# Optimization experiments

Measured on AMD Instinct MI355X. Metric: run time of the kernel, lower is better.

The kernel has to match this reference:

```python
import jax, jax.numpy as jnp
import numpy as np

H = 128
T = 120
F_IN = 180
BN_EPS = 1e-5
LEAKY_SLOPE = 0.01


def _lstm_layer(x, wih, whh, bih, bhh):
    """Single LSTM layer. x: (B,T,D); wih:(4H,D), whh:(4H,H). PyTorch gate order i,f,g,o."""
    B = x.shape[0]
    # Precompute input projections for all timesteps: (B,T,4H)
    x_proj = jnp.einsum('btd,gd->btg', x, wih) + bih + bhh
    x_proj = jnp.transpose(x_proj, (1, 0, 2))  # (T,B,4H) for scan over time
    h0 = jnp.zeros((B, H), dtype=x.dtype)
    c0 = jnp.zeros((B, H), dtype=x.dtype)

    def step(carry, xt):
        h, c = carry
        gates = xt + h @ whh.T  # (B,4H)
        i, f, g, o = jnp.split(gates, 4, axis=-1)
        i = jax.nn.sigmoid(i)
        f = jax.nn.sigmoid(f)
        g = jnp.tanh(g)
        o = jax.nn.sigmoid(o)
        c = f * c + i * g
        h = o * jnp.tanh(c)
        return (h, c), h

    (_, _), hs = jax.lax.scan(step, (h0, c0), x_proj)  # hs: (T,B,H)
    return jnp.transpose(hs, (1, 0, 2))  # (B,T,H)


def setup_inputs() -> dict:
    key = jax.random.key(0)
    ks = jax.random.split(key, 16)
    B = 2048
    s = 0.1  # keep activations in a stable range
    inp = {
        'x': jax.random.normal(ks[0], (B, F_IN, T), jnp.float32),
        'fc_w': jax.random.normal(ks[1], (H, F_IN), jnp.float32) * s,
        'fc_b': jax.random.normal(ks[2], (H,), jnp.float32) * s,
        'bn_g': jax.random.uniform(ks[3], (H,), jnp.float32, 0.5, 1.5),
        'bn_b': jax.random.normal(ks[4], (H,), jnp.float32) * s,
        'bn_mean': jax.random.normal(ks[5], (H,), jnp.float32) * s,
        'bn_var': jax.random.uniform(ks[6], (H,), jnp.float32, 0.5, 1.5),
        'wih0': jax.random.normal(ks[7], (4 * H, H), jnp.float32) * s,
        'whh0': jax.random.normal(ks[8], (4 * H, H), jnp.float32) * s,
        'bih0': jax.random.normal(ks[9], (4 * H,), jnp.float32) * s,
        'bhh0': jax.random.normal(ks[10], (4 * H,), jnp.float32) * s,
        'wih1': jax.random.normal(ks[11], (4 * H, H), jnp.float32) * s,
        'whh1': jax.random.normal(ks[12], (4 * H, H), jnp.float32) * s,
        'bih1': jax.random.normal(ks[13], (4 * H,), jnp.float32) * s,
        'bhh1': jax.random.normal(ks[14], (4 * H,), jnp.float32) * s,
    }
    return inp


def reference(x, fc_w, fc_b, bn_g, bn_b, bn_mean, bn_var,
              wih0, whh0, bih0, bhh0, wih1, whh1, bih1, bhh1):
    # x.reshape(-1,180,120).permute(0,2,1) -> (B,120,180)
    h = jnp.transpose(x.reshape(-1, F_IN, T), (0, 2, 1)).reshape(-1, F_IN)
    # Linear + BatchNorm1d (eval mode) + LeakyReLU
    h = h @ fc_w.T + fc_b
    h = (h - bn_mean) * jax.lax.rsqrt(bn_var + BN_EPS) * bn_g + bn_b
    h = jnp.where(h >= 0, h, LEAKY_SLOPE * h)
    h = h.reshape(-1, T, H)
    # 2-layer LSTM, take last timestep
    h = _lstm_layer(h, wih0, whh0, bih0, bhh0)
    h = _lstm_layer(h, wih1, whh1, bih1, bhh1)
    return h[:, -1, :]
```

## Files before the change

### kernel.cpp

```cpp
#include <hip/hip_runtime.h>

#define T_STEPS 120
#define NF_IN   180
#define H_DIM   128
#define G_DIM   512
#define K_FC    192
#define HP      136

#define L2E      1.4426950408889634f
#define TWO_L2E  2.8853900817779268f

typedef __attribute__((ext_vector_type(8))) short short8;
typedef __attribute__((ext_vector_type(4))) float f32x4;

#define LDS_BARRIER() asm volatile("s_waitcnt lgkmcnt(0)\ns_barrier" ::: "memory")

#if __has_builtin(__builtin_amdgcn_exp2f)
#define EXP2(x) __builtin_amdgcn_exp2f(x)
#else
#define EXP2(x) __expf((x) * 0.6931471805599453f)
#endif

__device__ __forceinline__ f32x4 mfma16(short8 a, short8 b, f32x4 c) {
    return __builtin_amdgcn_mfma_f32_16x16x32_bf16(a, b, c, 0, 0, 0);
}

__device__ __forceinline__ short f2bf(float x) {
    union { float f; unsigned u; } v; v.f = x;
    unsigned r = v.u + 0x7fffu + ((v.u >> 16) & 1u);
    return (short)(r >> 16);
}

__device__ __forceinline__ float sig2(float y) {
    return __builtin_amdgcn_rcpf(1.f + EXP2(y));
}
__device__ __forceinline__ float tanh2(float y) {
    return 1.f - 2.f * __builtin_amdgcn_rcpf(1.f + EXP2(y));
}

__global__ void prep_kernel(
    const float* __restrict__ fc_w, const float* __restrict__ fc_b,
    const float* __restrict__ bn_g, const float* __restrict__ bn_b,
    const float* __restrict__ bn_mean, const float* __restrict__ bn_var,
    const float* __restrict__ wih0, const float* __restrict__ whh0,
    const float* __restrict__ bih0, const float* __restrict__ bhh0,
    const float* __restrict__ wih1, const float* __restrict__ whh1,
    const float* __restrict__ bih1, const float* __restrict__ bhh1,
    short* __restrict__ fcw_o, float* __restrict__ fcb_o,
    float* __restrict__ bias0_o, float* __restrict__ bias1_o,
    short* __restrict__ wih0_o, short* __restrict__ whh0_o,
    short* __restrict__ wih1_o, short* __restrict__ whh1_o)
{
    int tid = blockIdx.x * blockDim.x + threadIdx.x;
    int stride = gridDim.x * blockDim.x;
    for (int i = tid; i < H_DIM * K_FC; i += stride) {
        int h = i / K_FC, f = i % K_FC;
        float s = bn_g[h] * rsqrtf(bn_var[h] + 1e-5f);
        float v = (f < NF_IN) ? fc_w[h * NF_IN + f] * s : 0.f;
        fcw_o[i] = f2bf(v);
    }
    for (int i = tid; i < H_DIM; i += stride) {
        float s = bn_g[i] * rsqrtf(bn_var[i] + 1e-5f);
        fcb_o[i] = (fc_b[i] - bn_mean[i]) * s + bn_b[i];
    }
    for (int i = tid; i < G_DIM; i += stride) {
        float sc = ((i >> 7) == 2) ? TWO_L2E : -L2E;
        bias0_o[i] = (bih0[i] + bhh0[i]) * sc;
        bias1_o[i] = (bih1[i] + bhh1[i]) * sc;
    }
    for (int i = tid; i < G_DIM * H_DIM; i += stride) {
        float sc = ((i >> 7) / H_DIM == 2) ? TWO_L2E : -L2E;
        wih0_o[i] = f2bf(wih0[i] * sc); whh0_o[i] = f2bf(whh0[i] * sc);
        wih1_o[i] = f2bf(wih1[i] * sc); whh1_o[i] = f2bf(whh1[i] * sc);
    }
}

__global__ __launch_bounds__(256) void fc_kernel(
    const float* __restrict__ x, const short* __restrict__ fcw,
    const float* __restrict__ fcb, short* __restrict__ xfc)
{
    __shared__ short outs[120 * 132];
    const int b = blockIdx.x;
    const int tid = threadIdx.x;
    const int wave = tid >> 6, lane = tid & 63;
    const int m16 = lane & 15, q = lane >> 4;

    short8 af[2][6];
#pragma unroll
    for (int mi = 0; mi < 2; ++mi) {
        int t = (wave * 2 + mi) * 16 + m16;
        if (t > 119) t = 119;
        const float* xb = x + (size_t)b * (NF_IN * T_STEPS) + (size_t)q * 8 * T_STEPS + t;
#pragma unroll
        for (int kc = 0; kc < 6; ++kc) {
            union { short s[8]; short8 v; } u;
#pragma unroll
            for (int j = 0; j < 8; ++j) {
                int f = kc * 32 + q * 8 + j;
                float val = (f < NF_IN) ? xb[(kc * 32 + j) * T_STEPS] : 0.f;
                u.s[j] = f2bf(val);
            }
            af[mi][kc] = u.v;
        }
    }

    float fcb_v[8];
#pragma unroll
    for (int nt = 0; nt < 8; ++nt) fcb_v[nt] = fcb[nt * 16 + m16];

    f32x4 acc[2][8];
#pragma unroll
    for (int mi = 0; mi < 2; ++mi)
#pragma unroll
        for (int nt = 0; nt < 8; ++nt) acc[mi][nt] = (f32x4){0.f, 0.f, 0.f, 0.f};

#pragma unroll
    for (int nt = 0; nt < 8; ++nt) {
        short8 bf[6];
#pragma unroll
        for (int kc = 0; kc < 6; ++kc)
            bf[kc] = *(const short8*)(fcw + (nt * 16 + m16) * K_FC + kc * 32 + q * 8);
#pragma unroll
        for (int mi = 0; mi < 2; ++mi)
#pragma unroll
            for (int kc = 0; kc < 6; ++kc)
                acc[mi][nt] = mfma16(af[mi][kc], bf[kc], acc[mi][nt]);
    }

#pragma unroll
    for (int mi = 0; mi < 2; ++mi)
#pragma unroll
        for (int nt = 0; nt < 8; ++nt)
#pragma unroll
            for (int r = 0; r < 4; ++r) {
                int t = (wave * 2 + mi) * 16 + q * 4 + r;
                int h = nt * 16 + m16;
                float v = acc[mi][nt][r] + fcb_v[nt];
                v = (v >= 0.f) ? v : 0.01f * v;
                if (t < 120) outs[t * 132 + h] = f2bf(v);
            }
    __syncthreads();

    unsigned* dst = (unsigned*)xfc + (size_t)b * (T_STEPS * H_DIM / 2);
    const unsigned* srcs = (const unsigned*)outs;
    for (int i = tid; i < T_STEPS * H_DIM / 2; i += 256) {
        int t = i >> 6, c2 = i & 63;
        dst[i] = srcs[t * 66 + c2];
    }
}

__global__ __launch_bounds__(512, 2) void lstm_kernel(
    const short* h_in, const short* __restrict__ wih,
    const short* __restrict__ whh, const float* __restrict__ bias,
    short* h_out, float* __restrict__ fout)
{
    __shared__ short h_lds[2 * 8 * HP];

    const int tid = threadIdx.x;
    const int w = tid >> 6, lane = tid & 63;
    const int m16 = lane & 15, q = lane >> 4, m8 = m16 & 7;
    const int b0 = blockIdx.x * 8;

    for (int i = tid; i < 8 * HP; i += 512) ((unsigned*)h_lds)[i] = 0u;

    short8 whf[4][4], wif[4][4];
    float bias_v[4];
#pragma unroll
    for (int g = 0; g < 4; ++g) {
        int n = g * 128 + w * 16 + m16;
        bias_v[g] = bias[n];
#pragma unroll
        for (int kc = 0; kc < 4; ++kc) {
            whf[g][kc] = *(const short8*)(whh + n * H_DIM + kc * 32 + q * 8);
            wif[g][kc] = *(const short8*)(wih + n * H_DIM + kc * 32 + q * 8);
        }
    }

    float c[4] = {0.f, 0.f, 0.f, 0.f};
    f32x4 P[4];
    f32x4 xps[4];

    auto loadPair = [&](short8 ax[4], int t1) {
        int t = t1 + (m16 >> 3);
        if (t > T_STEPS - 1) t = T_STEPS - 1;
        const short* src = h_in + ((size_t)(b0 + m8) * T_STEPS + t) * H_DIM + q * 8;
#pragma unroll
        for (int kc = 0; kc < 4; ++kc) ax[kc] = *(const short8*)(src + kc * 32);
    };

    auto projPairR = [&](const short8 ax[4]) {
#pragma unroll
        for (int g = 0; g < 4; ++g) {
            float bv = bias_v[g];
            f32x4 acc = (f32x4){bv, bv, bv, bv};
#pragma unroll
            for (int kc = 0; kc < 4; ++kc) acc = mfma16(ax[kc], wif[g][kc], acc);
            P[g] = acc;
        }
    };

    auto recUpdate = [&](int s, int rb, int hb, const f32x4 xp0, const f32x4 xp1,
                         const f32x4 xp2, const f32x4 xp3) {
        const short* rbp = h_lds + rb * (8 * HP) + m8 * HP + q * 8;
        short8 ar[4];
#pragma unroll
        for (int kc = 0; kc < 4; ++kc) ar[kc] = *(const short8*)(rbp + kc * 32);
        f32x4 a0 = xp0, a1 = xp1, a2 = xp2, a3 = xp3;
#pragma unroll
        for (int kc = 0; kc < 4; ++kc) {
            a0 = mfma16(ar[kc], whf[0][kc], a0);
            a1 = mfma16(ar[kc], whf[1][kc], a1);
            a2 = mfma16(ar[kc], whf[2][kc], a2);
            a3 = mfma16(ar[kc], whf[3][kc], a3);
        }
        float hv[4];
#pragma unroll
        for (int r = 0; r < 4; ++r) {
            float i_ = sig2(a0[r]);
            float f_ = sig2(a1[r]);
            float g_ = __builtin_fmaf(-2.f * TWO_L2E,
                                      __builtin_amdgcn_rcpf(1.f + EXP2(a2[r])),
                                      TWO_L2E);
            float o_ = sig2(a3[r]);
            c[r] = f_ * c[r] + i_ * g_;
            hv[r] = o_ * tanh2(c[r]);
        }
        const int dim = w * 16 + m16;
        if (q < 2) {
            short* hw = h_lds + hb * (8 * HP) + (q * 4) * HP + dim;
#pragma unroll
            for (int r = 0; r < 4; ++r) hw[r * HP] = f2bf(hv[r]);
        }
        if (fout != nullptr && s == T_STEPS - 1 && q < 2) {
#pragma unroll
            for (int r = 0; r < 4; ++r)
                fout[(size_t)(b0 + q * 4 + r) * H_DIM + dim] = hv[r];
        }
    };

    auto exportH = [&](int s, int hb) {
        int row = tid >> 6, c2 = tid & 63;
        unsigned v = ((const unsigned*)h_lds)[hb * (4 * HP) + row * (HP / 2) + c2];
        ((unsigned*)h_out)[((size_t)(b0 + row) * T_STEPS + s) * (H_DIM / 2) + c2] = v;
    };

    {
        short8 ax0[4];
        const short* src = h_in + (size_t)(b0 + m8) * T_STEPS * H_DIM + q * 8;
#pragma unroll
        for (int kc = 0; kc < 4; ++kc) ax0[kc] = *(const short8*)(src + kc * 32);
        projPairR(ax0);
    }
#pragma unroll
    for (int g = 0; g < 4; ++g) xps[g] = P[g];
    short8 axc[4];
    loadPair(axc, 1);
    LDS_BARRIER();

    for (int it = 0; it < T_STEPS / 2; ++it) {
        const int s = 2 * it;
        recUpdate(s, 1, 0, xps[0], xps[1], xps[2], xps[3]);
        projPairR(axc);
#pragma unroll
        for (int g = 0; g < 4; ++g)
#pragma unroll
            for (int e = 0; e < 4; ++e)
                xps[g][e] = __shfl_xor(P[g][e], 32);
        short8 axn[4];
        loadPair(axn, s + 3);
        if (h_out != nullptr && s >= 1) exportH(s - 1, 1);
        LDS_BARRIER();
        recUpdate(s + 1, 0, 1, P[0], P[1], P[2], P[3]);
#pragma unroll
        for (int kc = 0; kc < 4; ++kc) axc[kc] = axn[kc];
        if (h_out != nullptr) exportH(s, 0);
        LDS_BARRIER();
    }
    if (h_out != nullptr) exportH(T_STEPS - 1, 1);
}

static constexpr size_t OFF_FCW  = 0;
static constexpr size_t OFF_FCB  = 49152;
static constexpr size_t OFF_B0   = 49664;
static constexpr size_t OFF_B1   = 51712;
static constexpr size_t OFF_WIH0 = 53760;
static constexpr size_t OFF_WHH0 = 184832;
static constexpr size_t OFF_WIH1 = 315904;
static constexpr size_t OFF_WHH1 = 446976;
static constexpr size_t OFF_BUFA = 578048;

extern "C" void kernel_launch(void* const* d_in, const int* in_sizes, int n_in,
                              void* d_out, int out_size, void* d_ws, size_t ws_size,
                              hipStream_t stream) {
    const float* x       = (const float*)d_in[0];
    const float* fc_w    = (const float*)d_in[1];
    const float* fc_b    = (const float*)d_in[2];
    const float* bn_g    = (const float*)d_in[3];
    const float* bn_b    = (const float*)d_in[4];
    const float* bn_mean = (const float*)d_in[5];
    const float* bn_var  = (const float*)d_in[6];
    const float* wih0    = (const float*)d_in[7];
    const float* whh0    = (const float*)d_in[8];
    const float* bih0    = (const float*)d_in[9];
    const float* bhh0    = (const float*)d_in[10];
    const float* wih1    = (const float*)d_in[11];
    const float* whh1    = (const float*)d_in[12];
    const float* bih1    = (const float*)d_in[13];
    const float* bhh1    = (const float*)d_in[14];

    const int B = in_sizes[0] / (NF_IN * T_STEPS);

    char* ws = (char*)d_ws;
    short* fcw   = (short*)(ws + OFF_FCW);
    float* fcb   = (float*)(ws + OFF_FCB);
    float* bias0 = (float*)(ws + OFF_B0);
    float* bias1 = (float*)(ws + OFF_B1);
    short* wih0b = (short*)(ws + OFF_WIH0);
    short* whh0b = (short*)(ws + OFF_WHH0);
    short* wih1b = (short*)(ws + OFF_WIH1);
    short* whh1b = (short*)(ws + OFF_WHH1);
    short* bufA  = (short*)(ws + OFF_BUFA);

    prep_kernel<<<256, 256, 0, stream>>>(
        fc_w, fc_b, bn_g, bn_b, bn_mean, bn_var,
        wih0, whh0, bih0, bhh0, wih1, whh1, bih1, bhh1,
        fcw, fcb, bias0, bias1, wih0b, whh0b, wih1b, whh1b);

    fc_kernel<<<B, 256, 0, stream>>>(x, fcw, fcb, bufA);

    lstm_kernel<<<B / 8, 512, 0, stream>>>(bufA, wih0b, whh0b, bias0, bufA, nullptr);
    lstm_kernel<<<B / 8, 512, 0, stream>>>(bufA, wih1b, whh1b, bias1, nullptr, (float*)d_out);
}
```

Baseline: 560.9 us.

## Fuse both LSTM layers into one wavefront-pipelined kernel with progress flags

Replaces the two sequential LSTM layer launches with a single kernel. Half the blocks run layer 0 and publish each hidden step to global memory, then bump a per-batch-group progress counter. The other half run layer 1, spin-waiting on that counter so the two layers overlap in time. Each block now handles 16 batch rows instead of 8, which uses the full MFMA M dimension and drops the pairwise shuffle trick. The design assumes all 256 blocks are co-resident; if they are not, the spin-waits could deadlock. It also adds atomic load/store traffic and polling overhead.

```diff
diff --git a/kernel.cpp b/kernel.cpp
--- a/kernel.cpp
+++ b/kernel.cpp
@@ -49,10 +49,12 @@
     short* __restrict__ fcw_o, float* __restrict__ fcb_o,
     float* __restrict__ bias0_o, float* __restrict__ bias1_o,
     short* __restrict__ wih0_o, short* __restrict__ whh0_o,
-    short* __restrict__ wih1_o, short* __restrict__ whh1_o)
+    short* __restrict__ wih1_o, short* __restrict__ whh1_o,
+    int* __restrict__ prog_o)
 {
     int tid = blockIdx.x * blockDim.x + threadIdx.x;
     int stride = gridDim.x * blockDim.x;
+    for (int i = tid; i < 256; i += stride) prog_o[i] = 0;
     for (int i = tid; i < H_DIM * K_FC; i += stride) {
         int h = i / K_FC, f = i % K_FC;
         float s = bn_g[h] * rsqrtf(bn_var[h] + 1e-5f);
@@ -149,19 +151,32 @@
     }
 }
 
-__global__ __launch_bounds__(512, 2) void lstm_kernel(
-    const short* h_in, const short* __restrict__ wih,
-    const short* __restrict__ whh, const float* __restrict__ bias,
-    short* h_out, float* __restrict__ fout)
+__global__ __launch_bounds__(512, 2) void lstm_fused_kernel(
+    const short* __restrict__ xfc,
+    short* hpub,
+    const short* __restrict__ wih0b, const short* __restrict__ whh0b,
+    const float* __restrict__ bias0,
+    const short* __restrict__ wih1b, const short* __restrict__ whh1b,
+    const float* __restrict__ bias1,
+    int* prog, float* __restrict__ fout)
 {
-    __shared__ short h_lds[2 * 8 * HP];
+    __shared__ short h_lds[2 * 16 * HP];
 
     const int tid = threadIdx.x;
     const int w = tid >> 6, lane = tid & 63;
-    const int m16 = lane & 15, q = lane >> 4, m8 = m16 & 7;
-    const int b0 = blockIdx.x * 8;
-
-    for (int i = tid; i < 8 * HP; i += 512) ((unsigned*)h_lds)[i] = 0u;
+    const int m16 = lane & 15, q = lane >> 4;
+    const int role = blockIdx.x >> 7;
+    const int pb   = blockIdx.x & 127;
+    const int b0   = pb * 16;
+
+    const short* wih  = role ? wih1b : wih0b;
+    const short* whh  = role ? whh1b : whh0b;
+    const float* bias = role ? bias1 : bias0;
+
+    for (int i = tid; i < 8 * HP; i += 512) {
+        ((unsigned*)h_lds)[i] = 0u;
+        ((unsigned*)h_lds)[i + 8 * HP] = 0u;
+    }
 
     short8 whf[4][4], wif[4][4];
     float bias_v[4];
@@ -178,17 +193,30 @@
 
     float c[4] = {0.f, 0.f, 0.f, 0.f};
     f32x4 P[4];
-    f32x4 xps[4];
-
-    auto loadPair = [&](short8 ax[4], int t1) {
-        int t = t1 + (m16 >> 3);
+    short8 axc[4], axn[4];
+
+    auto loadX = [&](short8 ax[4], int t) {
         if (t > T_STEPS - 1) t = T_STEPS - 1;
-        const short* src = h_in + ((size_t)(b0 + m8) * T_STEPS + t) * H_DIM + q * 8;
-#pragma unroll
-        for (int kc = 0; kc < 4; ++kc) ax[kc] = *(const short8*)(src + kc * 32);
-    };
-
-    auto projPairR = [&](const short8 ax[4]) {
+        if (!role) {
+            const short* src = xfc + ((size_t)(b0 + m16) * T_STEPS + t) * H_DIM + q * 8;
+#pragma unroll
+            for (int kc = 0; kc < 4; ++kc) ax[kc] = *(const short8*)(src + kc * 32);
+        } else {
+            const unsigned* src = (const unsigned*)hpub
+                + ((size_t)(b0 + m16) * T_STEPS + t) * (H_DIM / 2) + q * 4;
+#pragma unroll
+            for (int kc = 0; kc < 4; ++kc) {
+                union { unsigned u[4]; short8 v; } uu;
+#pragma unroll
+                for (int jj = 0; jj < 4; ++jj)
+                    uu.u[jj] = __hip_atomic_load(src + kc * 16 + jj,
+                                                 __ATOMIC_RELAXED, __HIP_MEMORY_SCOPE_AGENT);
+                ax[kc] = uu.v;
+            }
+        }
+    };
+
+    auto projP = [&](const short8 ax[4]) {
 #pragma unroll
         for (int g = 0; g < 4; ++g) {
             float bv = bias_v[g];
@@ -199,13 +227,12 @@
         }
     };
 
-    auto recUpdate = [&](int s, int rb, int hb, const f32x4 xp0, const f32x4 xp1,
-                         const f32x4 xp2, const f32x4 xp3) {
-        const short* rbp = h_lds + rb * (8 * HP) + m8 * HP + q * 8;
+    auto recUpdate = [&](int s, int rb, int hb) {
+        const short* rbp = h_lds + rb * (16 * HP) + m16 * HP + q * 8;
         short8 ar[4];
 #pragma unroll
         for (int kc = 0; kc < 4; ++kc) ar[kc] = *(const short8*)(rbp + kc * 32);
-        f32x4 a0 = xp0, a1 = xp1, a2 = xp2, a3 = xp3;
+        f32x4 a0 = P[0], a1 = P[1], a2 = P[2], a3 = P[3];
 #pragma unroll
         for (int kc = 0; kc < 4; ++kc) {
             a0 = mfma16(ar[kc], whf[0][kc], a0);
@@ -225,58 +252,71 @@
             c[r] = f_ * c[r] + i_ * g_;
             hv[r] = o_ * tanh2(c[r]);
         }
-        const int dim = w * 16 + m16;
-        if (q < 2) {
-            short* hw = h_lds + hb * (8 * HP) + (q * 4) * HP + dim;
-#pragma unroll
-            for (int r = 0; r < 4; ++r) hw[r * HP] = f2bf(hv[r]);
-        }
-        if (fout != nullptr && s == T_STEPS - 1 && q < 2) {
+        short* hw = h_lds + hb * (16 * HP) + (q * 4) * HP + (w * 16 + m16);
+#pragma unroll
+        for (int r = 0; r < 4; ++r) hw[r * HP] = f2bf(hv[r]);
+        if (role && s == T_STEPS - 1) {
 #pragma unroll
             for (int r = 0; r < 4; ++r)
-                fout[(size_t)(b0 + q * 4 + r) * H_DIM + dim] = hv[r];
+                fout[(size_t)(b0 + q * 4 + r) * H_DIM + w * 16 + m16] = hv[r];
         }
     };
 
     auto exportH = [&](int s, int hb) {
-        int row = tid >> 6, c2 = tid & 63;
-        unsigned v = ((const unsigned*)h_lds)[hb * (4 * HP) + row * (HP / 2) + c2];
-        ((unsigned*)h_out)[((size_t)(b0 + row) * T_STEPS + s) * (H_DIM / 2) + c2] = v;
-    };
-
-    {
-        short8 ax0[4];
-        const short* src = h_in + (size_t)(b0 + m8) * T_STEPS * H_DIM + q * 8;
-#pragma unroll
-        for (int kc = 0; kc < 4; ++kc) ax0[kc] = *(const short8*)(src + kc * 32);
-        projPairR(ax0);
-    }
-#pragma unroll
-    for (int g = 0; g < 4; ++g) xps[g] = P[g];
-    short8 axc[4];
-    loadPair(axc, 1);
+        const unsigned* srcu = (const unsigned*)h_lds + hb * (8 * HP);
+        unsigned* dstu = (unsigned*)hpub;
+#pragma unroll
+        for (int i = tid; i < 16 * 64; i += 512) {
+            int row = i >> 6, col = i & 63;
+            unsigned v = srcu[row * (HP / 2) + col];
+            __hip_atomic_store(dstu + ((size_t)(b0 + row) * T_STEPS + s) * 64 + col,
+                               v, __ATOMIC_RELAXED, __HIP_MEMORY_SCOPE_AGENT);
+        }
+    };
+
+    auto waitProg = [&](int target) {
+        if (target > 120) target = 120;
+        while (__hip_atomic_load(prog + pb, __ATOMIC_RELAXED,
+                                 __HIP_MEMORY_SCOPE_AGENT) < target)
+            __builtin_amdgcn_s_sleep(2);
+    };
+
+    if (!role) {
+        loadX(axn, 0); projP(axn);
+        loadX(axc, 1);
+    } else {
+        waitProg(1); loadX(axn, 0); projP(axn);
+        waitProg(2); loadX(axc, 1);
+    }
     LDS_BARRIER();
 
     for (int it = 0; it < T_STEPS / 2; ++it) {
         const int s = 2 * it;
-        recUpdate(s, 1, 0, xps[0], xps[1], xps[2], xps[3]);
-        projPairR(axc);
-#pragma unroll
-        for (int g = 0; g < 4; ++g)
-#pragma unroll
-            for (int e = 0; e < 4; ++e)
-                xps[g][e] = __shfl_xor(P[g][e], 32);
-        short8 axn[4];
-        loadPair(axn, s + 3);
-        if (h_out != nullptr && s >= 1) exportH(s - 1, 1);
+        recUpdate(s, 1, 0);
+        projP(axc);
+        if (!role) { if (s >= 1) exportH(s - 1, 1); }
+        else waitProg(s + 3);
+        loadX(axn, s + 2);
         LDS_BARRIER();
-        recUpdate(s + 1, 0, 1, P[0], P[1], P[2], P[3]);
-#pragma unroll
-        for (int kc = 0; kc < 4; ++kc) axc[kc] = axn[kc];
-        if (h_out != nullptr) exportH(s, 0);
+        recUpdate(s + 1, 0, 1);
+        projP(axn);
+        if (!role) exportH(s, 0);
+        else waitProg(s + 4);
+        loadX(axc, s + 3);
+        if (!role) asm volatile("s_waitcnt vmcnt(4)" ::: "memory");
         LDS_BARRIER();
-    }
-    if (h_out != nullptr) exportH(T_STEPS - 1, 1);
+        if (!role && tid == 0)
+            __hip_atomic_store(prog + pb, s + 1,
+                               __ATOMIC_RELAXED, __HIP_MEMORY_SCOPE_AGENT);
+    }
+    if (!role) {
+        exportH(T_STEPS - 1, 1);
+        asm volatile("s_waitcnt vmcnt(0)" ::: "memory");
+        LDS_BARRIER();
+        if (tid == 0)
+            __hip_atomic_store(prog + pb, 120,
+                               __ATOMIC_RELAXED, __HIP_MEMORY_SCOPE_AGENT);
+    }
 }
 
 static constexpr size_t OFF_FCW  = 0;
@@ -287,7 +327,8 @@
 static constexpr size_t OFF_WHH0 = 184832;
 static constexpr size_t OFF_WIH1 = 315904;
 static constexpr size_t OFF_WHH1 = 446976;
-static constexpr size_t OFF_BUFA = 578048;
+static constexpr size_t OFF_PROG = 578048;
+static constexpr size_t OFF_BUFA = 579072;
 
 extern "C" void kernel_launch(void* const* d_in, const int* in_sizes, int n_in,
                               void* d_out, int out_size, void* d_ws, size_t ws_size,
@@ -319,15 +360,17 @@
     short* whh0b = (short*)(ws + OFF_WHH0);
     short* wih1b = (short*)(ws + OFF_WIH1);
     short* whh1b = (short*)(ws + OFF_WHH1);
+    int*   prog  = (int*)  (ws + OFF_PROG);
     short* bufA  = (short*)(ws + OFF_BUFA);
 
     prep_kernel<<<256, 256, 0, stream>>>(
         fc_w, fc_b, bn_g, bn_b, bn_mean, bn_var,
         wih0, whh0, bih0, bhh0, wih1, whh1, bih1, bhh1,
-        fcw, fcb, bias0, bias1, wih0b, whh0b, wih1b, whh1b);
+        fcw, fcb, bias0, bias1, wih0b, whh0b, wih1b, whh1b, prog);
 
     fc_kernel<<<B, 256, 0, stream>>>(x, fcw, fcb, bufA);
 
-    lstm_kernel<<<B / 8, 512, 0, stream>>>(bufA, wih0b, whh0b, bias0, bufA, nullptr);
-    lstm_kernel<<<B / 8, 512, 0, stream>>>(bufA, wih1b, whh1b, bias1, nullptr, (float*)d_out);
-}
+    lstm_fused_kernel<<<(B / 16) * 2, 512, 0, stream>>>(
+        bufA, bufA, wih0b, whh0b, bias0, wih1b, whh1b, bias1,
+        prog, (float*)d_out);
+}
```

Result: slower. 874.3 us (+55.9%).

## Split LSTM block into recurrent and input-projection wave groups via LDS

Applied to the files above, without the earlier changes.

Doubles the LSTM block to 1024 threads. Eight waves do only the recurrent h·Whh update, and eight producer waves compute the input projections for future timesteps into a 4-slot LDS ring and handle the h export. This takes the input-projection MFMAs, shuffles and global loads off the serial recurrent critical path and halves per-thread weight registers. In exchange it uses about 96KB of extra LDS per block, which likely limits occupancy to one block per CU, and it adds LDS round-trips for the projections.

```diff
diff --git a/kernel.cpp b/kernel.cpp
--- a/kernel.cpp
+++ b/kernel.cpp
@@ -6,6 +6,7 @@
 #define G_DIM   512
 #define K_FC    192
 #define HP      136
+#define XPR     12
 
 #define L2E      1.4426950408889634f
 #define TWO_L2E  2.8853900817779268f
@@ -149,69 +150,76 @@
     }
 }
 
-__global__ __launch_bounds__(512, 2) void lstm_kernel(
+__global__ __launch_bounds__(1024) void lstm_kernel(
     const short* h_in, const short* __restrict__ wih,
     const short* __restrict__ whh, const float* __restrict__ bias,
     short* h_out, float* __restrict__ fout)
 {
+    __shared__ float xp_lds[4][4][H_DIM * XPR];
     __shared__ short h_lds[2 * 8 * HP];
 
     const int tid = threadIdx.x;
     const int w = tid >> 6, lane = tid & 63;
     const int m16 = lane & 15, q = lane >> 4, m8 = m16 & 7;
+    const int wd = w & 7;
+    const bool isRec = (w < 8);
     const int b0 = blockIdx.x * 8;
-
-    for (int i = tid; i < 8 * HP; i += 512) ((unsigned*)h_lds)[i] = 0u;
-
-    short8 whf[4][4], wif[4][4];
+    const int dim = wd * 16 + m16;
+    const int rowb = (q & 1) * 4;
+
+    for (int i = tid; i < 8 * HP; i += 1024) ((unsigned*)h_lds)[i] = 0u;
+
+    short8 wf[4][4];
     float bias_v[4];
+    const short* wsrc = isRec ? whh : wih;
 #pragma unroll
     for (int g = 0; g < 4; ++g) {
-        int n = g * 128 + w * 16 + m16;
+        int n = g * 128 + dim;
         bias_v[g] = bias[n];
 #pragma unroll
-        for (int kc = 0; kc < 4; ++kc) {
-            whf[g][kc] = *(const short8*)(whh + n * H_DIM + kc * 32 + q * 8);
-            wif[g][kc] = *(const short8*)(wih + n * H_DIM + kc * 32 + q * 8);
-        }
+        for (int kc = 0; kc < 4; ++kc)
+            wf[g][kc] = *(const short8*)(wsrc + n * H_DIM + kc * 32 + q * 8);
     }
 
     float c[4] = {0.f, 0.f, 0.f, 0.f};
-    f32x4 P[4];
-    f32x4 xps[4];
-
-    auto loadPair = [&](short8 ax[4], int t1) {
+    short8 ab[4];
+
+    auto loadPair = [&](int t1) {
         int t = t1 + (m16 >> 3);
         if (t > T_STEPS - 1) t = T_STEPS - 1;
         const short* src = h_in + ((size_t)(b0 + m8) * T_STEPS + t) * H_DIM + q * 8;
 #pragma unroll
-        for (int kc = 0; kc < 4; ++kc) ax[kc] = *(const short8*)(src + kc * 32);
+        for (int kc = 0; kc < 4; ++kc) ab[kc] = *(const short8*)(src + kc * 32);
     };
 
-    auto projPairR = [&](const short8 ax[4]) {
-#pragma unroll
-        for (int g = 0; g < 4; ++g) {
+    auto projHalf = [&](int t1, int g0) {
+        const int slot = (t1 + (q >> 1)) & 3;
+#pragma unroll
+        for (int gg = 0; gg < 2; ++gg) {
+            int g = g0 + gg;
             float bv = bias_v[g];
             f32x4 acc = (f32x4){bv, bv, bv, bv};
 #pragma unroll
-            for (int kc = 0; kc < 4; ++kc) acc = mfma16(ax[kc], wif[g][kc], acc);
-            P[g] = acc;
+            for (int kc = 0; kc < 4; ++kc) acc = mfma16(ab[kc], wf[g][kc], acc);
+            *(f32x4*)&xp_lds[slot][g][dim * XPR + rowb] = acc;
         }
     };
 
-    auto recUpdate = [&](int s, int rb, int hb, const f32x4 xp0, const f32x4 xp1,
-                         const f32x4 xp2, const f32x4 xp3) {
+    auto recPhase = [&](int s, int rb, int hb) {
+        const int slot = s & 3;
+        f32x4 a0 = *(const f32x4*)&xp_lds[slot][0][dim * XPR + rowb];
+        f32x4 a1 = *(const f32x4*)&xp_lds[slot][1][dim * XPR + rowb];
+        f32x4 a2 = *(const f32x4*)&xp_lds[slot][2][dim * XPR + rowb];
+        f32x4 a3 = *(const f32x4*)&xp_lds[slot][3][dim * XPR + rowb];
         const short* rbp = h_lds + rb * (8 * HP) + m8 * HP + q * 8;
-        short8 ar[4];
-#pragma unroll
-        for (int kc = 0; kc < 4; ++kc) ar[kc] = *(const short8*)(rbp + kc * 32);
-        f32x4 a0 = xp0, a1 = xp1, a2 = xp2, a3 = xp3;
+#pragma unroll
+        for (int kc = 0; kc < 4; ++kc) ab[kc] = *(const short8*)(rbp + kc * 32);
 #pragma unroll
         for (int kc = 0; kc < 4; ++kc) {
-            a0 = mfma16(ar[kc], whf[0][kc], a0);
-            a1 = mfma16(ar[kc], whf[1][kc], a1);
-            a2 = mfma16(ar[kc], whf[2][kc], a2);
-            a3 = mfma16(ar[kc], whf[3][kc], a3);
+            a0 = mfma16(ab[kc], wf[0][kc], a0);
+            a1 = mfma16(ab[kc], wf[1][kc], a1);
+            a2 = mfma16(ab[kc], wf[2][kc], a2);
+            a3 = mfma16(ab[kc], wf[3][kc], a3);
         }
         float hv[4];
 #pragma unroll
@@ -225,58 +233,52 @@
             c[r] = f_ * c[r] + i_ * g_;
             hv[r] = o_ * tanh2(c[r]);
         }
-        const int dim = w * 16 + m16;
         if (q < 2) {
             short* hw = h_lds + hb * (8 * HP) + (q * 4) * HP + dim;
 #pragma unroll
             for (int r = 0; r < 4; ++r) hw[r * HP] = f2bf(hv[r]);
-        }
-        if (fout != nullptr && s == T_STEPS - 1 && q < 2) {
-#pragma unroll
-            for (int r = 0; r < 4; ++r)
-                fout[(size_t)(b0 + q * 4 + r) * H_DIM + dim] = hv[r];
+            if (fout != nullptr && s == T_STEPS - 1) {
+#pragma unroll
+                for (int r = 0; r < 4; ++r)
+                    fout[(size_t)(b0 + q * 4 + r) * H_DIM + dim] = hv[r];
+            }
         }
     };
 
     auto exportH = [&](int s, int hb) {
-        int row = tid >> 6, c2 = tid & 63;
+        int pt = tid & 511;
+        int row = pt >> 6, c2 = pt & 63;
         unsigned v = ((const unsigned*)h_lds)[hb * (4 * HP) + row * (HP / 2) + c2];
         ((unsigned*)h_out)[((size_t)(b0 + row) * T_STEPS + s) * (H_DIM / 2) + c2] = v;
     };
 
-    {
-        short8 ax0[4];
-        const short* src = h_in + (size_t)(b0 + m8) * T_STEPS * H_DIM + q * 8;
-#pragma unroll
-        for (int kc = 0; kc < 4; ++kc) ax0[kc] = *(const short8*)(src + kc * 32);
-        projPairR(ax0);
-    }
-#pragma unroll
-    for (int g = 0; g < 4; ++g) xps[g] = P[g];
-    short8 axc[4];
-    loadPair(axc, 1);
+    if (!isRec) {
+        loadPair(0);
+        projHalf(0, 0);
+        projHalf(0, 2);
+        loadPair(2);
+    }
     LDS_BARRIER();
 
     for (int it = 0; it < T_STEPS / 2; ++it) {
         const int s = 2 * it;
-        recUpdate(s, 1, 0, xps[0], xps[1], xps[2], xps[3]);
-        projPairR(axc);
-#pragma unroll
-        for (int g = 0; g < 4; ++g)
-#pragma unroll
-            for (int e = 0; e < 4; ++e)
-                xps[g][e] = __shfl_xor(P[g][e], 32);
-        short8 axn[4];
-        loadPair(axn, s + 3);
-        if (h_out != nullptr && s >= 1) exportH(s - 1, 1);
+        if (isRec) {
+            recPhase(s, 1, 0);
+        } else {
+            projHalf(s + 2, 0);
+            if (h_out != nullptr && s >= 1) exportH(s - 1, 1);
+        }
         LDS_BARRIER();
-        recUpdate(s + 1, 0, 1, P[0], P[1], P[2], P[3]);
-#pragma unroll
-        for (int kc = 0; kc < 4; ++kc) axc[kc] = axn[kc];
-        if (h_out != nullptr) exportH(s, 0);
+        if (isRec) {
+            recPhase(s + 1, 0, 1);
+        } else {
+            projHalf(s + 2, 2);
+            if (h_out != nullptr) exportH(s, 0);
+            loadPair(s + 4);
+        }
         LDS_BARRIER();
     }
-    if (h_out != nullptr) exportH(T_STEPS - 1, 1);
+    if (!isRec && h_out != nullptr) exportH(T_STEPS - 1, 1);
 }
 
 static constexpr size_t OFF_FCW  = 0;
@@ -328,6 +330,6 @@
 
     fc_kernel<<<B, 256, 0, stream>>>(x, fcw, fcb, bufA);
 
-    lstm_kernel<<<B / 8, 512, 0, stream>>>(bufA, wih0b, whh0b, bias0, bufA, nullptr);
-    lstm_kernel<<<B / 8, 512, 0, stream>>>(bufA, wih1b, whh1b, bias1, nullptr, (float*)d_out);
-}
+    lstm_kernel<<<B / 8, 1024, 0, stream>>>(bufA, wih0b, whh0b, bias0, bufA, nullptr);
+    lstm_kernel<<<B / 8, 1024, 0, stream>>>(bufA, wih1b, whh1b, bias1, nullptr, (float*)d_out);
+}
```

Result: slower. 632.6 us (+12.8%).
